# Optimization experiments

Measured on AMD Instinct MI355X. Metric: run time of the kernel, lower is better.

The kernel has to match this reference:

```python
import jax, jax.numpy as jnp
import numpy as np

N = 100000   # active voxels
K = 27       # 3x3x3 kernel offsets
C = 64       # in_channels == out_channels (residual block)
EPS = 1e-5


def setup_inputs() -> dict:
    key = jax.random.key(0)
    ks = jax.random.split(key, 10)
    feats = jax.random.normal(ks[0], (N, C), dtype=jnp.float32)
    # kernel-map: for each voxel, index of the neighbor voxel for each of the 27 offsets
    nbr = jax.random.randint(ks[1], (N, K), 0, N)
    nbr = nbr.at[:, K // 2].set(jnp.arange(N))  # center offset is identity
    w_scale = 1.0 / np.sqrt(K * C)
    W1 = jax.random.normal(ks[2], (K, C, C), dtype=jnp.float32) * w_scale
    b1 = jax.random.normal(ks[3], (C,), dtype=jnp.float32) * 0.01
    g1 = jnp.ones((C,), jnp.float32)
    be1 = jnp.zeros((C,), jnp.float32)
    W2 = jax.random.normal(ks[4], (K, C, C), dtype=jnp.float32) * w_scale
    b2 = jax.random.normal(ks[5], (C,), dtype=jnp.float32) * 0.01
    g2 = jnp.ones((C,), jnp.float32)
    be2 = jnp.zeros((C,), jnp.float32)
    return {"feats": feats, "nbr": nbr, "W1": W1, "b1": b1, "g1": g1, "be1": be1,
            "W2": W2, "b2": b2, "g2": g2, "be2": be2}


def _sparse_conv(f, nbr, W, b):
    # gather neighbor features per kernel offset: [N, K, C]
    g = f[nbr]
    # per-offset matmul and reduce over offsets (gather-matmul-scatter form)
    return jnp.einsum('nkc,kcd->nd', g, W) + b


def _bn(x, gamma, beta):
    # BatchNorm over active voxels (training-mode batch stats, per channel)
    mu = x.mean(axis=0)
    var = x.var(axis=0)
    return (x - mu) * jax.lax.rsqrt(var + EPS) * gamma + beta


def reference(feats, nbr, W1, b1, g1, be1, W2, b2, g2, be2):
    h = jax.nn.relu(_bn(_sparse_conv(feats, nbr, W1, b1), g1, be1))
    h = _bn(_sparse_conv(h, nbr, W2, b2), g2, be2)
    return jax.nn.relu(h + feats)  # residual add + ReLU
```

## Files before the change

### kernel.cpp

```cpp
#include <hip/hip_runtime.h>

#define NCH 64
#define KOFF 27
#define EPSV 1e-5f

typedef __attribute__((ext_vector_type(8))) short  bf16x8;
typedef __attribute__((ext_vector_type(4))) float  f32x4;
typedef __attribute__((ext_vector_type(8))) unsigned short u16x8;

__device__ __forceinline__ unsigned short f2bf(float x) {
    unsigned int u = __float_as_uint(x);
    u += 0x7fffu + ((u >> 16) & 1u);
    return (unsigned short)(u >> 16);
}

__global__ __launch_bounds__(256)
void prep_kernel(const float* __restrict__ feats,
                 const float* __restrict__ W1, const float* __restrict__ W2,
                 unsigned short* __restrict__ fbf,
                 unsigned short* __restrict__ wt1, unsigned short* __restrict__ wt2,
                 float* __restrict__ stat, int total8)
{
    const int b = blockIdx.x;
    if (b == 0) {
        stat[threadIdx.x] = 0.f;
        return;
    }
    if (b <= 108) {
        const float* W = (b <= 54) ? W1 : W2;
        unsigned short* Wt = (b <= 54) ? wt1 : wt2;
        const int t = (b <= 54 ? b - 1 : b - 55) * 256 + threadIdx.x;
        const int l  = t & 63;
        const int ct = (t >> 6) & 3;
        const int s  = (t >> 8) & 1;
        const int k  = t >> 9;
        const int d     = ct * 16 + (l & 15);
        const int cbase = s * 32 + (l >> 4) * 8;
        u16x8 o;
#pragma unroll
        for (int j = 0; j < 8; ++j)
            o[j] = f2bf(W[(size_t)k * 4096 + (size_t)(cbase + j) * 64 + d]);
        reinterpret_cast<u16x8*>(Wt)[t] = o;
        return;
    }
    const int idx = (b - 109) * 256 + threadIdx.x;
    if (idx >= total8) return;
    const float4* xp = reinterpret_cast<const float4*>(feats) + (size_t)idx * 2;
    const float4 a = xp[0], c = xp[1];
    u16x8 o;
    o[0] = f2bf(a.x); o[1] = f2bf(a.y); o[2] = f2bf(a.z); o[3] = f2bf(a.w);
    o[4] = f2bf(c.x); o[5] = f2bf(c.y); o[6] = f2bf(c.z); o[7] = f2bf(c.w);
    reinterpret_cast<u16x8*>(fbf)[idx] = o;
}

__global__ __launch_bounds__(256, 2)
void conv_mfma_kernel(const unsigned short* __restrict__ fin,
                      const int* __restrict__ nbr,
                      const unsigned short* __restrict__ Wt,
                      const float* __restrict__ bias,
                      float* __restrict__ out, float* __restrict__ pstat, int N)
{
    __shared__ int            s_idx[128 * KOFF];
    __shared__ unsigned short s_w[6 * 4096];

    const int lane = threadIdx.x & 63;
    const int wv   = threadIdx.x >> 6;
    const int n0   = blockIdx.x * 128;
    const int m    = lane & 15;
    const int quad = lane >> 4;

    {
        const int rem  = N - n0;
        const int maxi = (rem < 128 ? rem : 128) * KOFF;
        const int* nb  = nbr + (size_t)n0 * KOFF;
        for (int p = threadIdx.x; p < 128 * KOFF; p += 256)
            s_idx[p] = ((p < maxi) ? nb[p] : 0) * (NCH * 2);
    }

    f32x4 acc[2][4];
#pragma unroll
    for (int mt = 0; mt < 2; ++mt)
#pragma unroll
        for (int ct = 0; ct < 4; ++ct) acc[mt][ct] = (f32x4){0.f, 0.f, 0.f, 0.f};

    bf16x8 A[2][2][2];
    bf16x8 B[2][4];
    const char* finB = (const char*)fin;
    const int lv0 = wv * 32;

#define LOADA(kk, p)                                                         \
    {                                                                        \
        _Pragma("unroll")                                                    \
        for (int mt = 0; mt < 2; ++mt) {                                     \
            const int ofs = s_idx[(lv0 + mt * 16 + m) * KOFF + (kk)];        \
            const char* fp = finB + ofs + quad * 16;                         \
            A[p][mt][0] = *reinterpret_cast<const bf16x8*>(fp);              \
            A[p][mt][1] = *reinterpret_cast<const bf16x8*>(fp + 64);         \
        }                                                                    \
    }

#define LOADB_LDS(kk)                                                        \
    {                                                                        \
        const unsigned short* wp = s_w + (kk) * 4096 + lane * 8;             \
        _Pragma("unroll")                                                    \
        for (int s = 0; s < 2; ++s)                                          \
            _Pragma("unroll")                                                \
            for (int ct = 0; ct < 4; ++ct)                                   \
                B[s][ct] =                                                   \
                    *reinterpret_cast<const bf16x8*>(wp + (s * 4 + ct) * 512);\
    }

#define DOMFMA(p)                                                            \
    {                                                                        \
        _Pragma("unroll")                                                    \
        for (int mt = 0; mt < 2; ++mt)                                       \
            _Pragma("unroll")                                                \
            for (int s = 0; s < 2; ++s)                                      \
                _Pragma("unroll")                                            \
                for (int ct = 0; ct < 4; ++ct)                               \
                    acc[mt][ct] = __builtin_amdgcn_mfma_f32_16x16x32_bf16(   \
                        A[p][mt][s], B[s][ct], acc[mt][ct], 0, 0, 0);        \
    }

#pragma unroll 1
    for (int c = 0; c < 5; ++c) {
        const int kb  = c * 6;
        const int len = (KOFF - kb < 6) ? (KOFF - kb) : 6;

        {
            const u16x8* gw = reinterpret_cast<const u16x8*>(
                Wt + (size_t)kb * 4096);
            u16x8* lw = reinterpret_cast<u16x8*>(s_w);
            const int units = len * 512;
#pragma unroll
            for (int i = 0; i < 12; ++i) {
                const int u = threadIdx.x + i * 256;
                if (u < units) lw[u] = gw[u];
            }
        }
        LOADA(kb, 0);
        __syncthreads();

        int kk = 0;
#pragma unroll 1
        for (; kk + 2 < len; kk += 2) {
            LOADA(kb + kk + 1, 1);
            LOADB_LDS(kk);
            __builtin_amdgcn_sched_barrier(0);
            DOMFMA(0);
            LOADA(kb + kk + 2, 0);
            LOADB_LDS(kk + 1);
            __builtin_amdgcn_sched_barrier(0);
            DOMFMA(1);
        }
        if (kk + 1 < len) {
            LOADA(kb + kk + 1, 1);
            LOADB_LDS(kk);
            __builtin_amdgcn_sched_barrier(0);
            DOMFMA(0);
            LOADB_LDS(kk + 1);
            __builtin_amdgcn_sched_barrier(0);
            DOMFMA(1);
        } else {
            LOADB_LDS(kk);
            __builtin_amdgcn_sched_barrier(0);
            DOMFMA(0);
        }
        __syncthreads();
    }
#undef LOADA
#undef LOADB_LDS
#undef DOMFMA

#pragma unroll
    for (int ct = 0; ct < 4; ++ct) {
        const int ch = ct * 16 + m;
        const float bv = bias[ch];
        float s = 0.f, q = 0.f;
#pragma unroll
        for (int mt = 0; mt < 2; ++mt) {
#pragma unroll
            for (int r = 0; r < 4; ++r) {
                const int vox = n0 + lv0 + mt * 16 + quad * 4 + r;
                if (vox < N) {
                    const float v = acc[mt][ct][r] + bv;
                    out[(size_t)vox * NCH + ch] = v;
                    s += v;
                    q += v * v;
                }
            }
        }
        s += __shfl_xor(s, 16, 64);
        s += __shfl_xor(s, 32, 64);
        q += __shfl_xor(q, 16, 64);
        q += __shfl_xor(q, 32, 64);
        if (quad == 0) {
            float* pr = pstat + ((size_t)blockIdx.x * 4 + wv) * 128;
            pr[ch]      = s;
            pr[64 + ch] = q;
        }
    }
}

__global__ __launch_bounds__(256)
void reduce_stats_kernel(const float* __restrict__ pstat, float* __restrict__ stat,
                         int rows)
{
    __shared__ float s_[256];
    const int ch = threadIdx.x & 127;
    const int h  = threadIdx.x >> 7;
    float acc = 0.f;
    for (int r = blockIdx.x * 2 + h; r < rows; r += gridDim.x * 2)
        acc += pstat[(size_t)r * 128 + ch];
    s_[threadIdx.x] = acc;
    __syncthreads();
    if (threadIdx.x < 128)
        atomicAdd(&stat[threadIdx.x], s_[threadIdx.x] + s_[threadIdx.x + 128]);
}

__global__ __launch_bounds__(256)
void bn_relu_bf16_kernel(const float* __restrict__ x, const float* __restrict__ sums,
                         const float* __restrict__ gmm, const float* __restrict__ bet,
                         float invN, unsigned short* __restrict__ y, int total8)
{
    const int idx = blockIdx.x * 256 + threadIdx.x;
    if (idx >= total8) return;
    const int c0 = (idx & 7) * 8;
    const float4* xp = reinterpret_cast<const float4*>(x) + (size_t)idx * 2;
    const float4 a = xp[0], b = xp[1];
    float v[8] = {a.x, a.y, a.z, a.w, b.x, b.y, b.z, b.w};
    u16x8 o;
#pragma unroll
    for (int i = 0; i < 8; ++i) {
        const int c = c0 + i;
        const float mu  = sums[c] * invN;
        const float var = sums[64 + c] * invN - mu * mu;
        const float rs  = rsqrtf(var + EPSV);
        const float sc  = gmm[c] * rs;
        const float sh  = bet[c] - mu * sc;
        o[i] = f2bf(fmaxf(fmaf(v[i], sc, sh), 0.f));
    }
    reinterpret_cast<u16x8*>(y)[idx] = o;
}

__global__ __launch_bounds__(256)
void bn_res_relu_kernel(float* __restrict__ x, const float* __restrict__ feats,
                        const float* __restrict__ sums, const float* __restrict__ gmm,
                        const float* __restrict__ bet, float invN, int total4)
{
    const int idx = blockIdx.x * blockDim.x + threadIdx.x;
    if (idx >= total4) return;
    float4 v = reinterpret_cast<float4*>(x)[idx];
    const float4 f = reinterpret_cast<const float4*>(feats)[idx];
    const int c0 = (idx & 15) * 4;
    float sc[4], sh[4];
#pragma unroll
    for (int i = 0; i < 4; ++i) {
        const int c = c0 + i;
        const float mu  = sums[c] * invN;
        const float var = sums[64 + c] * invN - mu * mu;
        const float rs  = rsqrtf(var + EPSV);
        sc[i] = gmm[c] * rs;
        sh[i] = bet[c] - mu * sc[i];
    }
    v.x = fmaxf(fmaf(v.x, sc[0], sh[0]) + f.x, 0.f);
    v.y = fmaxf(fmaf(v.y, sc[1], sh[1]) + f.y, 0.f);
    v.z = fmaxf(fmaf(v.z, sc[2], sh[2]) + f.z, 0.f);
    v.w = fmaxf(fmaf(v.w, sc[3], sh[3]) + f.w, 0.f);
    reinterpret_cast<float4*>(x)[idx] = v;
}

extern "C" void kernel_launch(void* const* d_in, const int* in_sizes, int n_in,
                              void* d_out, int out_size, void* d_ws, size_t ws_size,
                              hipStream_t stream)
{
    const float* feats = (const float*)d_in[0];
    const int*   nbr   = (const int*)d_in[1];
    const float* W1    = (const float*)d_in[2];
    const float* b1    = (const float*)d_in[3];
    const float* g1    = (const float*)d_in[4];
    const float* be1   = (const float*)d_in[5];
    const float* W2    = (const float*)d_in[6];
    const float* b2    = (const float*)d_in[7];
    const float* g2    = (const float*)d_in[8];
    const float* be2   = (const float*)d_in[9];
    float* out = (float*)d_out;

    const int N  = in_sizes[0] / NCH;
    const int NC = N * NCH;
    const float invN = 1.0f / (float)N;

    float*          h0   = (float*)d_ws;
    unsigned short* fbf  = (unsigned short*)(h0 + NC);
    unsigned short* hbf  = fbf + NC;
    unsigned short* wt1  = hbf + NC;
    unsigned short* wt2  = wt1 + KOFF * 4096;
    float*          stat = (float*)(wt2 + KOFF * 4096);

    const int total8   = NC / 8;
    const int castGrid = (total8 + 255) / 256;
    const int prepGrid = 1 + 108 + castGrid;
    const int convGrid = (N + 127) / 128;
    const int statRows = convGrid * 4;

    float* pstat1 = out;
    float* pstat2 = h0;

    prep_kernel<<<prepGrid, 256, 0, stream>>>(feats, W1, W2, fbf, wt1, wt2,
                                              stat, total8);
    conv_mfma_kernel<<<convGrid, 256, 0, stream>>>(fbf, nbr, wt1, b1, h0,
                                                   pstat1, N);
    reduce_stats_kernel<<<32, 256, 0, stream>>>(pstat1, stat, statRows);
    bn_relu_bf16_kernel<<<castGrid, 256, 0, stream>>>(h0, stat, g1, be1, invN,
                                                      hbf, total8);
    conv_mfma_kernel<<<convGrid, 256, 0, stream>>>(hbf, nbr, wt2, b2, out,
                                                   pstat2, N);
    reduce_stats_kernel<<<32, 256, 0, stream>>>(pstat2, stat + 128, statRows);
    bn_res_relu_kernel<<<(NC / 4 + 255) / 256, 256, 0, stream>>>(
        out, feats, stat + 128, g2, be2, invN, NC / 4);
}
```

Measured before the change: 326.4 us.

## Shrink weight LDS stage to 3 offsets and raise occupancy to 4 blocks

Cuts the per-block LDS weight buffer from 6 to 3 kernel offsets and raises the launch-bounds minimum blocks per CU from 2 to 4, so more waves can hide gather latency. The offset loop is fully unrolled into 9 chunks of 3, with double-buffered A gathers prefetched across chunk boundaries. This adds more barriers and weight reloads per block, and the tighter register budget risks spills.

Measured after the change: 286.3 us. 1.14x faster.

```diff
diff --git a/kernel.cpp b/kernel.cpp
--- a/kernel.cpp
+++ b/kernel.cpp
@@ -53,7 +53,7 @@
     reinterpret_cast<u16x8*>(fbf)[idx] = o;
 }
 
-__global__ __launch_bounds__(256, 2)
+__global__ __launch_bounds__(256, 4)
 void conv_mfma_kernel(const unsigned short* __restrict__ fin,
                       const int* __restrict__ nbr,
                       const unsigned short* __restrict__ Wt,
@@ -61,7 +61,7 @@
                       float* __restrict__ out, float* __restrict__ pstat, int N)
 {
     __shared__ int            s_idx[128 * KOFF];
-    __shared__ unsigned short s_w[6 * 4096];
+    __shared__ unsigned short s_w[3 * 4096];
 
     const int lane = threadIdx.x & 63;
     const int wv   = threadIdx.x >> 6;
@@ -76,6 +76,7 @@
         for (int p = threadIdx.x; p < 128 * KOFF; p += 256)
             s_idx[p] = ((p < maxi) ? nb[p] : 0) * (NCH * 2);
     }
+    __syncthreads();
 
     f32x4 acc[2][4];
 #pragma unroll
@@ -88,14 +89,14 @@
     const char* finB = (const char*)fin;
     const int lv0 = wv * 32;
 
-#define LOADA(kk, p)                                                         \
+#define LOADA(kk)                                                            \
     {                                                                        \
         _Pragma("unroll")                                                    \
         for (int mt = 0; mt < 2; ++mt) {                                     \
             const int ofs = s_idx[(lv0 + mt * 16 + m) * KOFF + (kk)];        \
             const char* fp = finB + ofs + quad * 16;                         \
-            A[p][mt][0] = *reinterpret_cast<const bf16x8*>(fp);              \
-            A[p][mt][1] = *reinterpret_cast<const bf16x8*>(fp + 64);         \
+            A[(kk) & 1][mt][0] = *reinterpret_cast<const bf16x8*>(fp);       \
+            A[(kk) & 1][mt][1] = *reinterpret_cast<const bf16x8*>(fp + 64);  \
         }                                                                    \
     }
 
@@ -110,7 +111,7 @@
                     *reinterpret_cast<const bf16x8*>(wp + (s * 4 + ct) * 512);\
     }
 
-#define DOMFMA(p)                                                            \
+#define DOMFMA(kk)                                                           \
     {                                                                        \
         _Pragma("unroll")                                                    \
         for (int mt = 0; mt < 2; ++mt)                                       \
@@ -119,53 +120,40 @@
                 _Pragma("unroll")                                            \
                 for (int ct = 0; ct < 4; ++ct)                               \
                     acc[mt][ct] = __builtin_amdgcn_mfma_f32_16x16x32_bf16(   \
-                        A[p][mt][s], B[s][ct], acc[mt][ct], 0, 0, 0);        \
-    }
-
-#pragma unroll 1
-    for (int c = 0; c < 5; ++c) {
-        const int kb  = c * 6;
-        const int len = (KOFF - kb < 6) ? (KOFF - kb) : 6;
+                        A[(kk) & 1][mt][s], B[s][ct], acc[mt][ct], 0, 0, 0); \
+    }
+
+    LOADA(0);
+
+#pragma unroll
+    for (int c = 0; c < 9; ++c) {
+        const int kb = c * 3;
 
         {
             const u16x8* gw = reinterpret_cast<const u16x8*>(
                 Wt + (size_t)kb * 4096);
             u16x8* lw = reinterpret_cast<u16x8*>(s_w);
-            const int units = len * 512;
-#pragma unroll
-            for (int i = 0; i < 12; ++i) {
-                const int u = threadIdx.x + i * 256;
-                if (u < units) lw[u] = gw[u];
-            }
+#pragma unroll
+            for (int i = 0; i < 6; ++i)
+                lw[threadIdx.x + i * 256] = gw[threadIdx.x + i * 256];
         }
-        LOADA(kb, 0);
         __syncthreads();
 
-        int kk = 0;
-#pragma unroll 1
-        for (; kk + 2 < len; kk += 2) {
-            LOADA(kb + kk + 1, 1);
-            LOADB_LDS(kk);
-            __builtin_amdgcn_sched_barrier(0);
-            DOMFMA(0);
-            LOADA(kb + kk + 2, 0);
-            LOADB_LDS(kk + 1);
-            __builtin_amdgcn_sched_barrier(0);
-            DOMFMA(1);
-        }
-        if (kk + 1 < len) {
-            LOADA(kb + kk + 1, 1);
-            LOADB_LDS(kk);
-            __builtin_amdgcn_sched_barrier(0);
-            DOMFMA(0);
-            LOADB_LDS(kk + 1);
-            __builtin_amdgcn_sched_barrier(0);
-            DOMFMA(1);
-        } else {
-            LOADB_LDS(kk);
-            __builtin_amdgcn_sched_barrier(0);
-            DOMFMA(0);
-        }
+        LOADA(kb + 1);
+        LOADB_LDS(0);
+        __builtin_amdgcn_sched_barrier(0);
+        DOMFMA(kb);
+
+        LOADA(kb + 2);
+        LOADB_LDS(1);
+        __builtin_amdgcn_sched_barrier(0);
+        DOMFMA(kb + 1);
+
+        if (c < 8) LOADA(kb + 3);
+        LOADB_LDS(2);
+        __builtin_amdgcn_sched_barrier(0);
+        DOMFMA(kb + 2);
+
         __syncthreads();
     }
 #undef LOADA
```
